# Kernel optimization log

Measured on AMD Instinct MI355X. Metric: run time of the kernel, lower is better.

The kernel has to match this reference:

```python
import jax, jax.numpy as jnp
import numpy as np

FACTOR = 5

def setup_inputs() -> dict:
    key = jax.random.key(0)
    k1, k2, k3 = jax.random.split(key, 3)
    B, L, H, D = 4, 2048, 8, 64
    logL = int(np.ceil(np.log(L)))          # 8
    U_part = min(2 * FACTOR * logL, L)      # 80 sampled keys per query
    queries = jax.random.normal(k1, (B, L, H, D), dtype=jnp.float32)
    keys = jax.random.normal(k2, (B, L, H, D), dtype=jnp.float32)
    index_sample = jax.random.randint(k3, (L, U_part), 0, L)
    return {"queries": queries, "keys": keys, "index_sample": index_sample}

def reference(queries, keys, index_sample):
    B, L, H, D = queries.shape
    q = jnp.transpose(queries, (0, 2, 1, 3))   # [B,H,L,D]
    k = jnp.transpose(keys, (0, 2, 1, 3))      # [B,H,L,D]
    logL = int(np.ceil(np.log(L)))
    u = min(FACTOR * logL, L)                  # n_top queries

    # sample keys per query position: [B,H,L,S,D]
    K_sample = k[:, :, index_sample, :]
    # Q_i . K_sample_ij : [B,H,L,S]
    QK_sample = jnp.einsum('bhld,bhlsd->bhls', q, K_sample)
    # sparsity measure M = max - mean (mean over full L as in source)
    M = QK_sample.max(axis=-1) - QK_sample.sum(axis=-1) / L   # [B,H,L]
    _, M_top = jax.lax.top_k(M, u)                            # [B,H,u]

    # gather selected queries and compute full scores against all keys
    Q_reduce = jnp.take_along_axis(q, M_top[..., None], axis=2)  # [B,H,u,D]
    scale = 1.0 / jnp.sqrt(jnp.float32(D))
    scores = jnp.einsum('bhud,bhld->bhul', Q_reduce, k) * scale  # [B,H,u,L]
    attn = jax.nn.softmax(scores, axis=-1)

    # scatter softmaxed rows into full [B,H,L,L] attention matrix (rest zeros)
    out = jnp.zeros((B, H, L, L), dtype=attn.dtype)
    b_idx = jnp.arange(B)[:, None, None]
    h_idx = jnp.arange(H)[None, :, None]
    out = out.at[b_idx, h_idx, M_top, :].set(attn)
    return out
```

## Files before the change

kernel.cpp:

```cpp
#include <hip/hip_runtime.h>
#include <math.h>

#define NB 4
#define NL 2048
#define NH 8
#define ND 64
#define NUPART 80
#define NUTOP 40

__global__ __launch_bounds__(256) void k_compute_M_zero(
    const float* __restrict__ q, const float* __restrict__ k,
    const int* __restrict__ idx, float* __restrict__ M,
    float4* __restrict__ outz)
{
    const int t    = threadIdx.x;
    const int w    = blockIdx.x * 4 + (t >> 6);
    const int lane = t & 63;
    const int l    = w & (NL - 1);
    const int bh   = w >> 11;
    const int h    = bh & (NH - 1);
    const int b    = bh >> 3;
    const int sl   = lane >> 2;
    const int dg   = lane & 3;
    const int d0   = dg * 16;

    {
        float4* o = outz + (size_t)blockIdx.x * 2048 + t;
        const float4 z = make_float4(0.f, 0.f, 0.f, 0.f);
#pragma unroll
        for (int j = 0; j < 8; ++j) o[j * 256] = z;
    }

    const float4* qv = (const float4*)(q + (((size_t)(b * NL + l) * NH + h) * ND + d0));
    const float4 q0 = qv[0], q1 = qv[1], q2 = qv[2], q3 = qv[3];

    float mx = -INFINITY, sm = 0.0f;
#pragma unroll
    for (int r = 0; r < 5; ++r) {
        const int s  = r * 16 + sl;
        const int ki = idx[l * NUPART + s];
        const float4* kv = (const float4*)(k + (((size_t)(b * NL + ki) * NH + h) * ND + d0));
        const float4 k0 = kv[0], k1 = kv[1], k2 = kv[2], k3 = kv[3];
        float p = q0.x * k0.x + q0.y * k0.y + q0.z * k0.z + q0.w * k0.w
                + q1.x * k1.x + q1.y * k1.y + q1.z * k1.z + q1.w * k1.w
                + q2.x * k2.x + q2.y * k2.y + q2.z * k2.z + q2.w * k2.w
                + q3.x * k3.x + q3.y * k3.y + q3.z * k3.z + q3.w * k3.w;
        p += __shfl_xor(p, 1);
        p += __shfl_xor(p, 2);
        mx = fmaxf(mx, p);
        sm += p;
    }
#pragma unroll
    for (int m = 4; m < 64; m <<= 1) {
        mx = fmaxf(mx, __shfl_xor(mx, m));
        sm += __shfl_xor(sm, m);
    }
    if (lane == 0) M[w] = mx - sm * (1.0f / (float)NL);
}

__global__ __launch_bounds__(256) void k_topk(
    const float* __restrict__ M, int* __restrict__ Mtop)
{
    __shared__ float sM[NL];
    __shared__ float rv[4];
    __shared__ int   ri[4];
    const int bh = blockIdx.x;
    const int t  = threadIdx.x;

    for (int j = t; j < NL; j += 256) sM[j] = M[bh * NL + j];
    __syncthreads();

    for (int it = 0; it < NUTOP; ++it) {
        float v = -INFINITY;
        int   i = NL;
        for (int j = t; j < NL; j += 256) {
            const float m = sM[j];
            if (m > v || (m == v && j < i)) { v = m; i = j; }
        }
#pragma unroll
        for (int off = 1; off < 64; off <<= 1) {
            const float ov = __shfl_xor(v, off);
            const int   oi = __shfl_xor(i, off);
            if (ov > v || (ov == v && oi < i)) { v = ov; i = oi; }
        }
        const int wid = t >> 6;
        if ((t & 63) == 0) { rv[wid] = v; ri[wid] = i; }
        __syncthreads();
        if (t == 0) {
            for (int w2 = 1; w2 < 4; ++w2) {
                if (rv[w2] > v || (rv[w2] == v && ri[w2] < i)) { v = rv[w2]; i = ri[w2]; }
            }
            Mtop[bh * NUTOP + it] = i;
            sM[i] = -INFINITY;
        }
        __syncthreads();
    }
}

__global__ __launch_bounds__(256) void k_attn(
    const float* __restrict__ q, const float* __restrict__ k,
    const int* __restrict__ Mtop, float* __restrict__ out)
{
    __shared__ float redm[4];
    __shared__ float reds[4];

    const int bh  = blockIdx.x / NUTOP;
    const int ui  = blockIdx.x % NUTOP;
    const int b   = bh >> 3;
    const int h   = bh & 7;
    const int row = Mtop[bh * NUTOP + ui];
    const int t   = threadIdx.x;
    const int lane = t & 63;
    const int wid  = t >> 6;

    const float4* qv = (const float4*)(q + (((size_t)(b * NL + row)) * NH + h) * ND);
    float4 qr[16];
#pragma unroll
    for (int i = 0; i < 16; ++i) qr[i] = qv[i];

    float sc[8];
    float mx = -INFINITY;
#pragma unroll
    for (int j = 0; j < 8; ++j) {
        const int l = t + 256 * j;
        const float4* kv = (const float4*)(k + (((size_t)(b * NL + l)) * NH + h) * ND);
        float s = 0.0f;
#pragma unroll
        for (int i = 0; i < 16; ++i) {
            const float4 kk = kv[i];
            s += qr[i].x * kk.x + qr[i].y * kk.y + qr[i].z * kk.z + qr[i].w * kk.w;
        }
        sc[j] = s * 0.125f;
        mx = fmaxf(mx, sc[j]);
    }

#pragma unroll
    for (int off = 1; off < 64; off <<= 1) mx = fmaxf(mx, __shfl_xor(mx, off));
    if (lane == 0) redm[wid] = mx;
    __syncthreads();
    mx = fmaxf(fmaxf(redm[0], redm[1]), fmaxf(redm[2], redm[3]));

    float lsum = 0.0f;
#pragma unroll
    for (int j = 0; j < 8; ++j) {
        sc[j] = __expf(sc[j] - mx);
        lsum += sc[j];
    }
#pragma unroll
    for (int off = 1; off < 64; off <<= 1) lsum += __shfl_xor(lsum, off);
    if (lane == 0) reds[wid] = lsum;
    __syncthreads();
    const float inv = 1.0f / (reds[0] + reds[1] + reds[2] + reds[3]);

    float* orow = out + ((size_t)bh * NL + row) * NL;
#pragma unroll
    for (int j = 0; j < 8; ++j) {
        orow[t + 256 * j] = sc[j] * inv;
    }
}

extern "C" void kernel_launch(void* const* d_in, const int* in_sizes, int n_in,
                              void* d_out, int out_size, void* d_ws, size_t ws_size,
                              hipStream_t stream) {
    const float* q   = (const float*)d_in[0];
    const float* k   = (const float*)d_in[1];
    const int*   idx = (const int*)d_in[2];
    float* out = (float*)d_out;

    float* Mws  = (float*)d_ws;
    int*   Mtop = (int*)((char*)d_ws + (size_t)NB * NH * NL * 4);

    k_compute_M_zero<<<NB * NH * NL / 4, 256, 0, stream>>>(q, k, idx, Mws, (float4*)out);
    k_topk<<<NB * NH, 256, 0, stream>>>(Mws, Mtop);
    k_attn<<<NB * NH * NUTOP, 256, 0, stream>>>(q, k, Mtop, out);
}
```

Measured before the change: 385.8 us.

## Split output zero-fill between M kernel and attention kernel, skipping selected rows

The first kernel now zeroes only the first 1800 rows of each head's output matrix instead of all of it. The remaining 248 rows are zeroed by the attention kernel, which skips any row that top-k marked as selected using a new rowmap array. This trims zero-store traffic that would be overwritten anyway and moves part of the fill into the lighter attention launch. In exchange it adds rowmap writes in the top-k kernel and a per-row flag check, and it adds a dependency on fixed row ranges hard-coded to these dimensions.

```diff
diff --git a/kernel.cpp b/kernel.cpp
--- a/kernel.cpp
+++ b/kernel.cpp
@@ -7,13 +7,27 @@
 #define ND 64
 #define NUPART 80
 #define NUTOP 40
+#define ZROWS1 1800
+
+typedef float vfloat4 __attribute__((ext_vector_type(4)));
 
 __global__ __launch_bounds__(256) void k_compute_M_zero(
     const float* __restrict__ q, const float* __restrict__ k,
     const int* __restrict__ idx, float* __restrict__ M,
-    float4* __restrict__ outz)
+    float* __restrict__ out)
 {
-    const int t    = threadIdx.x;
+    const int t = threadIdx.x;
+
+    {
+        const int bhz = blockIdx.x >> 9;
+        const int j   = blockIdx.x & 511;
+        vfloat4* o = (vfloat4*)out + (size_t)bhz * (NL * (ND * 8)) + j * 1800 + t;
+        const vfloat4 z = (vfloat4)(0.0f);
+#pragma unroll
+        for (int i = 0; i < 7; ++i) o[i * 256] = z;
+        if (t < 8) o[7 * 256] = z;
+    }
+
     const int w    = blockIdx.x * 4 + (t >> 6);
     const int lane = t & 63;
     const int l    = w & (NL - 1);
@@ -23,13 +37,6 @@
     const int sl   = lane >> 2;
     const int dg   = lane & 3;
     const int d0   = dg * 16;
-
-    {
-        float4* o = outz + (size_t)blockIdx.x * 2048 + t;
-        const float4 z = make_float4(0.f, 0.f, 0.f, 0.f);
-#pragma unroll
-        for (int j = 0; j < 8; ++j) o[j * 256] = z;
-    }
 
     const float4* qv = (const float4*)(q + (((size_t)(b * NL + l) * NH + h) * ND + d0));
     const float4 q0 = qv[0], q1 = qv[1], q2 = qv[2], q3 = qv[3];
@@ -59,7 +66,8 @@
 }
 
 __global__ __launch_bounds__(256) void k_topk(
-    const float* __restrict__ M, int* __restrict__ Mtop)
+    const float* __restrict__ M, int* __restrict__ rowmap,
+    int* __restrict__ Mtop)
 {
     __shared__ float sM[NL];
     __shared__ float rv[4];
@@ -67,7 +75,10 @@
     const int bh = blockIdx.x;
     const int t  = threadIdx.x;
 
-    for (int j = t; j < NL; j += 256) sM[j] = M[bh * NL + j];
+    for (int j = t; j < NL; j += 256) {
+        sM[j] = M[bh * NL + j];
+        rowmap[bh * NL + j] = 0;
+    }
     __syncthreads();
 
     for (int it = 0; it < NUTOP; ++it) {
@@ -91,25 +102,41 @@
                 if (rv[w2] > v || (rv[w2] == v && ri[w2] < i)) { v = rv[w2]; i = ri[w2]; }
             }
             Mtop[bh * NUTOP + it] = i;
+            rowmap[bh * NL + i] = 1;
             sM[i] = -INFINITY;
         }
         __syncthreads();
     }
 }
 
-__global__ __launch_bounds__(256) void k_attn(
+__global__ __launch_bounds__(256) void k_attn_zero(
     const float* __restrict__ q, const float* __restrict__ k,
-    const int* __restrict__ Mtop, float* __restrict__ out)
+    const int* __restrict__ rowmap, const int* __restrict__ Mtop,
+    float* __restrict__ out)
 {
-    __shared__ float redm[4];
-    __shared__ float reds[4];
-
     const int bh  = blockIdx.x / NUTOP;
     const int ui  = blockIdx.x % NUTOP;
     const int b   = bh >> 3;
     const int h   = bh & 7;
+    const int t   = threadIdx.x;
     const int row = Mtop[bh * NUTOP + ui];
-    const int t   = threadIdx.x;
+
+    {
+        const vfloat4 z = (vfloat4)(0.0f);
+        int r0, nr;
+        if (ui < 8) { r0 = ZROWS1 + ui * 7; nr = 7; }
+        else        { r0 = ZROWS1 + 56 + (ui - 8) * 6; nr = 6; }
+        for (int rr = 0; rr < nr; ++rr) {
+            const int rz = r0 + rr;
+            if (rowmap[bh * NL + rz]) continue;
+            vfloat4* o = (vfloat4*)out + ((size_t)bh * NL + rz) * (NL / 4) + t;
+            o[0]   = z;
+            o[256] = z;
+        }
+    }
+
+    __shared__ float redm[4];
+    __shared__ float reds[4];
     const int lane = t & 63;
     const int wid  = t >> 6;
 
@@ -167,10 +194,11 @@
     const int*   idx = (const int*)d_in[2];
     float* out = (float*)d_out;
 
-    float* Mws  = (float*)d_ws;
-    int*   Mtop = (int*)((char*)d_ws + (size_t)NB * NH * NL * 4);
-
-    k_compute_M_zero<<<NB * NH * NL / 4, 256, 0, stream>>>(q, k, idx, Mws, (float4*)out);
-    k_topk<<<NB * NH, 256, 0, stream>>>(Mws, Mtop);
-    k_attn<<<NB * NH * NUTOP, 256, 0, stream>>>(q, k, Mtop, out);
-}
+    float* Mws    = (float*)d_ws;
+    int*   rowmap = (int*)((char*)d_ws + (size_t)NB * NH * NL * 4);
+    int*   Mtop   = (int*)((char*)d_ws + (size_t)NB * NH * NL * 8);
+
+    k_compute_M_zero<<<NB * NH * NL / 4, 256, 0, stream>>>(q, k, idx, Mws, out);
+    k_topk<<<NB * NH, 256, 0, stream>>>(Mws, rowmap, Mtop);
+    k_attn_zero<<<NB * NH * NUTOP, 256, 0, stream>>>(q, k, rowmap, Mtop, out);
+}
```

After: 379.4 us. No clear change (-1.6%).
